# Kernel optimization log

Measured on AMD Instinct MI355X. Metric: run time of the kernel, lower is better.

## Reference

```python
import jax, jax.numpy as jnp
import numpy as np

N = 100000
E = 1600000
D = 64
N_LAYERS = 2


def setup_inputs() -> dict:
    key = jax.random.key(0)
    ks = jax.random.split(key, 4 + 4 * N_LAYERS)
    h = jax.random.normal(ks[0], (N, D), dtype=jnp.float32)
    x = jax.random.normal(ks[1], (N, 3), dtype=jnp.float32)
    edge_index = jax.random.randint(ks[2], (2, E), 0, N, dtype=jnp.int64)
    node_mask = jnp.ones((N, 1), dtype=jnp.float32)
    scale = 1.0 / np.sqrt(D)
    params = {}
    for i in range(N_LAYERS):
        params[f'W1_{i}'] = jax.random.normal(ks[4 + 4 * i], (D, D), dtype=jnp.float32) * scale
        params[f'b1_{i}'] = jax.random.normal(ks[5 + 4 * i], (D,), dtype=jnp.float32) * scale
        params[f'W2_{i}'] = jax.random.normal(ks[6 + 4 * i], (D, D), dtype=jnp.float32) * scale
        params[f'b2_{i}'] = jax.random.normal(ks[7 + 4 * i], (D,), dtype=jnp.float32) * scale
    return dict(h=h, x=x, edge_index=edge_index, node_mask=node_mask, **params)


def _gin_layer(h, src, dst, W1, b1, W2, b2):
    # GINConv with eps=0: mlp(h_i + sum_{j->i} h_j)
    agg = jax.ops.segment_sum(h[src], dst, num_segments=N)  # [N, D]
    z = h + agg
    z = jax.nn.relu(z @ W1 + b1)
    return z @ W2 + b2


def reference(h, x, edge_index, node_mask,
              W1_0, b1_0, W2_0, b2_0,
              W1_1, b1_1, W2_1, b2_1):
    src, dst = edge_index[0], edge_index[1]
    h = _gin_layer(h, src, dst, W1_0, b1_0, W2_0, b2_0)
    h = _gin_layer(h, src, dst, W1_1, b1_1, W2_1, b2_1)
    h = h * node_mask
    return (h, x)
```

## Files before the change

kernel.cpp:

```cpp
#include <hip/hip_runtime.h>


#define NN 100000
#define EE 1600000
#define CAP 48
#define NBIN 1024
#define BINCAP 2688
#define CHB 6250
#define OVF_CAPN 8000

#define OVFC_OFF   1024
#define OVF_OFF    1026
#define CNT_OFF    19200
#define BUCK_OFF   119296
#define BINNED_OFF 4919296
#define HB_OFF     4919296
#define PW_OFF     8119328

typedef __attribute__((ext_vector_type(8))) short s8v;
typedef __attribute__((ext_vector_type(4))) float f4v;

union U8 { unsigned u[4]; s8v s; };

static __device__ __forceinline__ unsigned short f2bf(float f) {
  unsigned u = __float_as_uint(f);
  return (unsigned short)((u + 0x7FFF + ((u >> 16) & 1)) >> 16);
}
static __device__ __forceinline__ float bf2f(unsigned short s) {
  return __uint_as_float(((unsigned)s) << 16);
}
static __device__ __forceinline__ unsigned pk2(float lo, float hi) {
  return (unsigned)f2bf(lo) | ((unsigned)f2bf(hi) << 16);
}

__global__ __launch_bounds__(256) void setup_k(const float* __restrict__ W1a,
                                               const float* __restrict__ W2a,
                                               const float* __restrict__ W1b,
                                               const float* __restrict__ W2b,
                                               unsigned short* __restrict__ pw,
                                               int* __restrict__ wsp) {
  const int t = threadIdx.x;
#pragma unroll
  for (int i = t; i < NBIN; i += 256) wsp[i] = i * BINCAP;
  if (t == 0) wsp[OVFC_OFF] = 0;
  const float* Ws[4] = {W1a, W2a, W1b, W2b};
#pragma unroll
  for (int m = 0; m < 4; ++m) {
    const float* __restrict__ W = Ws[m];
#pragma unroll 1
    for (int i = 0; i < 16; ++i) {
      const int e = i * 256 + t;
      const int j = e & 7;
      const int lv = (e >> 3) & 63;
      const int ks = (e >> 9) & 1;
      const int tt = e >> 10;
      const int k = ks * 32 + (lv >> 4) * 8 + j;
      const int n = tt * 16 + (lv & 15);
      pw[m * 4096 + e] = f2bf(W[k * 64 + n]);
    }
  }
}

__global__ __launch_bounds__(256) void scatter_k(const int* __restrict__ src,
                                                 const int* __restrict__ dst,
                                                 int* __restrict__ gcur,
                                                 int* __restrict__ binned,
                                                 int* __restrict__ ovf) {
  __shared__ int hist[NBIN], base[NBIN], lcnt[NBIN];
  const int t = threadIdx.x;
#pragma unroll
  for (int b = t; b < NBIN; b += 256) { hist[b] = 0; lcnt[b] = 0; }
  __syncthreads();
  const int s = blockIdx.x * CHB;
#pragma unroll 1
  for (int p = t; p < CHB / 2; p += 256) {
    const int2 dd = *reinterpret_cast<const int2*>(dst + s + 2 * p);
    atomicAdd(&hist[dd.x >> 7], 1);
    atomicAdd(&hist[dd.y >> 7], 1);
  }
  __syncthreads();
#pragma unroll
  for (int b = t; b < NBIN; b += 256) {
    const int c = hist[b];
    base[b] = c ? atomicAdd(&gcur[b], c) : 0;
  }
  __syncthreads();
#pragma unroll 1
  for (int p = t; p < CHB / 2; p += 256) {
    const int i = s + 2 * p;
    const int2 dd = *reinterpret_cast<const int2*>(dst + i);
    const int2 ss = *reinterpret_cast<const int2*>(src + i);
    {
      const int bin = dd.x >> 7;
      const int slot = base[bin] + atomicAdd(&lcnt[bin], 1);
      if (slot < (bin + 1) * BINCAP) {
        binned[slot] = ((dd.x & 127) << 17) | ss.x;
      } else {
        const int q = atomicAdd(&ovf[-2], 1);
        if (q < OVF_CAPN) { ovf[2 * q] = dd.x; ovf[2 * q + 1] = ss.x; }
      }
    }
    {
      const int bin = dd.y >> 7;
      const int slot = base[bin] + atomicAdd(&lcnt[bin], 1);
      if (slot < (bin + 1) * BINCAP) {
        binned[slot] = ((dd.y & 127) << 17) | ss.y;
      } else {
        const int q = atomicAdd(&ovf[-2], 1);
        if (q < OVF_CAPN) { ovf[2 * q] = dd.y; ovf[2 * q + 1] = ss.y; }
      }
    }
  }
}

__global__ __launch_bounds__(256) void bucketize_k(const int* __restrict__ gcur,
                                                   const int* __restrict__ binned,
                                                   int* __restrict__ bucket,
                                                   int* __restrict__ cnt,
                                                   int* __restrict__ ovf) {
  __shared__ int c128[128];
  const int t = threadIdx.x;
  const int bin = blockIdx.x;
  const int nbase = bin << 7;
  if (t < 128) c128[t] = 0;
  __syncthreads();
  const int s0 = bin * BINCAP;
  const int s1 = min(gcur[bin], s0 + BINCAP);
#pragma unroll 1
  for (int i = s0 + t; i < s1; i += 256) {
    const int p = binned[i];
    const int dlow = p >> 17;
    const int sv = p & 131071;
    const int slot = atomicAdd(&c128[dlow], 1);
    if (slot < CAP) {
      bucket[(nbase + dlow) * CAP + slot] = sv;
    } else {
      const int q = atomicAdd(&ovf[-2], 1);
      if (q < OVF_CAPN) { ovf[2 * q] = nbase + dlow; ovf[2 * q + 1] = sv; }
    }
  }
  __syncthreads();
  if (t < 128 && nbase + t < NN) {
    const int dc = min(c128[t], CAP);
    cnt[nbase + t] = c128[t];
    const int pad = min((dc + 15) & ~15, CAP);
    int* __restrict__ brow = bucket + (nbase + t) * CAP;
#pragma unroll 1
    for (int q2 = dc; q2 < pad; ++q2) brow[q2] = NN;
  }
}

__global__ __launch_bounds__(256) void cvtx_k(const float* __restrict__ h,
                                              unsigned* __restrict__ hb,
                                              const float* __restrict__ x,
                                              float* __restrict__ ox) {
  const int b = blockIdx.x;
  const int t = threadIdx.x;
  if (b < 3125) {
    const int i = b * 256 + t;
    const float4* __restrict__ h4 = reinterpret_cast<const float4*>(h);
    const float4 a = h4[2 * i], c = h4[2 * i + 1];
    uint4 o;
    o.x = pk2(a.x, a.y); o.y = pk2(a.z, a.w);
    o.z = pk2(c.x, c.y); o.w = pk2(c.z, c.w);
    reinterpret_cast<uint4*>(hb)[i] = o;
  } else {
    if (b == 3125 && t < 32) hb[NN * 32 + t] = 0;
    const int i = (b - 3125) * 256 + t;
    if (i < (NN * 3) / 4)
      reinterpret_cast<float4*>(ox)[i] = reinterpret_cast<const float4*>(x)[i];
  }
}

__global__ __launch_bounds__(256) void agg_k(const unsigned short* __restrict__ hb,
                                             const int* __restrict__ cnt,
                                             const int* __restrict__ bucket,
                                             unsigned* __restrict__ zbu) {
  const int l = threadIdx.x & 63;
  const int s = l >> 4, g = l & 15;
  int nb = blockIdx.x * 8 + (threadIdx.x >> 6) * 2;
  nb = __builtin_amdgcn_readfirstlane(nb);
  const int n0 = nb, n1 = nb + 1;

  const int2 c2 = *reinterpret_cast<const int2*>(cnt + n0);
  const int deg0 = min(c2.x, CAP), deg1 = min(c2.y, CAP);
  const int nit0 = (deg0 + 15) >> 4, nit1 = (deg1 + 15) >> 4;
  const int nc = min(nit0, nit1);

  const int4* __restrict__ br0 = reinterpret_cast<const int4*>(bucket + n0 * CAP);
  const int4* __restrict__ br1 = reinterpret_cast<const int4*>(bucket + n1 * CAP);
  const uint2* __restrict__ h2 = reinterpret_cast<const uint2*>(hb);

  const uint2 sv0 = h2[n0 * 16 + g];
  const uint2 sv1 = h2[n1 * 16 + g];
  const unsigned p00 = (s == 0) ? sv0.x : 0u, p01 = (s == 0) ? sv0.y : 0u;
  const unsigned p10 = (s == 0) ? sv1.x : 0u, p11 = (s == 0) ? sv1.y : 0u;
  float a0 = __uint_as_float(p00 << 16), a1 = __uint_as_float(p00 & 0xffff0000u);
  float a2 = __uint_as_float(p01 << 16), a3 = __uint_as_float(p01 & 0xffff0000u);
  float b0 = __uint_as_float(p10 << 16), b1 = __uint_as_float(p10 & 0xffff0000u);
  float b2 = __uint_as_float(p11 << 16), b3 = __uint_as_float(p11 & 0xffff0000u);

#define ACCA(vv)                                   \
    a0 += __uint_as_float(vv.x << 16);             \
    a1 += __uint_as_float(vv.x & 0xffff0000u);     \
    a2 += __uint_as_float(vv.y << 16);             \
    a3 += __uint_as_float(vv.y & 0xffff0000u);
#define ACCB(vv)                                   \
    b0 += __uint_as_float(vv.x << 16);             \
    b1 += __uint_as_float(vv.x & 0xffff0000u);     \
    b2 += __uint_as_float(vv.y << 16);             \
    b3 += __uint_as_float(vv.y & 0xffff0000u);

#pragma unroll 1
  for (int it = 0; it < nc; ++it) {
    const int4 q0 = br0[it * 4 + s];
    const int4 q1 = br1[it * 4 + s];
    const uint2 v0 = h2[q0.x * 16 + g];
    const uint2 v1 = h2[q0.y * 16 + g];
    const uint2 v2 = h2[q0.z * 16 + g];
    const uint2 v3 = h2[q0.w * 16 + g];
    const uint2 w0 = h2[q1.x * 16 + g];
    const uint2 w1 = h2[q1.y * 16 + g];
    const uint2 w2 = h2[q1.z * 16 + g];
    const uint2 w3 = h2[q1.w * 16 + g];
    ACCA(v0) ACCA(v1) ACCA(v2) ACCA(v3)
    ACCB(w0) ACCB(w1) ACCB(w2) ACCB(w3)
  }
#pragma unroll 1
  for (int it = nc; it < nit0; ++it) {
    const int4 q0 = br0[it * 4 + s];
    const uint2 v0 = h2[q0.x * 16 + g];
    const uint2 v1 = h2[q0.y * 16 + g];
    const uint2 v2 = h2[q0.z * 16 + g];
    const uint2 v3 = h2[q0.w * 16 + g];
    ACCA(v0) ACCA(v1) ACCA(v2) ACCA(v3)
  }
#pragma unroll 1
  for (int it = nc; it < nit1; ++it) {
    const int4 q1 = br1[it * 4 + s];
    const uint2 w0 = h2[q1.x * 16 + g];
    const uint2 w1 = h2[q1.y * 16 + g];
    const uint2 w2 = h2[q1.z * 16 + g];
    const uint2 w3 = h2[q1.w * 16 + g];
    ACCB(w0) ACCB(w1) ACCB(w2) ACCB(w3)
  }
#undef ACCA
#undef ACCB

  a0 += __shfl_xor(a0, 16); a1 += __shfl_xor(a1, 16);
  a2 += __shfl_xor(a2, 16); a3 += __shfl_xor(a3, 16);
  a0 += __shfl_xor(a0, 32); a1 += __shfl_xor(a1, 32);
  a2 += __shfl_xor(a2, 32); a3 += __shfl_xor(a3, 32);
  b0 += __shfl_xor(b0, 16); b1 += __shfl_xor(b1, 16);
  b2 += __shfl_xor(b2, 16); b3 += __shfl_xor(b3, 16);
  b0 += __shfl_xor(b0, 32); b1 += __shfl_xor(b1, 32);
  b2 += __shfl_xor(b2, 32); b3 += __shfl_xor(b3, 32);

  if (s == 0) {
    uint2 o0, o1;
    o0.x = pk2(a0, a1); o0.y = pk2(a2, a3);
    o1.x = pk2(b0, b1); o1.y = pk2(b2, b3);
    reinterpret_cast<uint2*>(zbu)[n0 * 32 + g] = o0;
    reinterpret_cast<uint2*>(zbu)[n1 * 32 + g] = o1;
  }
}

__global__ __launch_bounds__(256) void ovf_fix_k(const unsigned short* __restrict__ hb,
                                                 char* __restrict__ zb,
                                                 const int* __restrict__ ovfCnt,
                                                 const int* __restrict__ ovf) {
  const int cv = min(ovfCnt[0], OVF_CAPN);
  const int l = threadIdx.x & 63;
  const int w = threadIdx.x >> 6;
  for (int p = w; p < cv; p += 4) {
    const int d = ovf[2 * p];
    const int s = ovf[2 * p + 1];
    const float add = bf2f(hb[(s << 6) | l]);
    unsigned* wp = reinterpret_cast<unsigned*>(zb + d * 256 + (l >> 1) * 4);
    const bool hi = l & 1;
    unsigned cur = atomicAdd(wp, 0u);
    while (true) {
      const unsigned short hv = hi ? (unsigned short)(cur >> 16) : (unsigned short)(cur & 0xffffu);
      const unsigned short nh = f2bf(bf2f(hv) + add);
      const unsigned nw = hi ? ((cur & 0x0000ffffu) | ((unsigned)nh << 16))
                             : ((cur & 0xffff0000u) | (unsigned)nh);
      const unsigned prev = atomicCAS(wp, cur, nw);
      if (prev == cur) break;
      cur = prev;
    }
  }
}

template <int OUTBF>
__global__ __launch_bounds__(256) void mlp_mfma_k(
    const char* __restrict__ zb,
    void* __restrict__ hout,
    const unsigned short* __restrict__ pw1, const float* __restrict__ b1,
    const unsigned short* __restrict__ pw2, const float* __restrict__ b2,
    const float* __restrict__ mask) {
  __shared__ unsigned ldsu[128 * 33];
  const int tid = threadIdx.x;
  const int w = tid >> 6, l = tid & 63, g = l >> 4, mi = l & 15;
  const int m0 = blockIdx.x * 128;
  const int rbase = w * 32;

  s8v zf[2][2];
#pragma unroll
  for (int tm = 0; tm < 2; ++tm) {
    const int node = m0 + rbase + tm * 16 + mi;
    const int nc = node < NN ? node : NN - 1;
#pragma unroll
    for (int ks = 0; ks < 2; ++ks)
      zf[tm][ks] = *reinterpret_cast<const s8v*>(zb + nc * 256 + (ks * 32 + g * 8) * 2);
  }

  f4v acc[4][2];
#pragma unroll
  for (int t = 0; t < 4; ++t) {
    const f4v bv = *reinterpret_cast<const f4v*>(b1 + t * 16 + g * 4);
    acc[t][0] = bv; acc[t][1] = bv;
  }
#pragma unroll
  for (int t = 0; t < 4; ++t) {
#pragma unroll
    for (int ks = 0; ks < 2; ++ks) {
      const s8v wf = *reinterpret_cast<const s8v*>(pw1 + ((t * 2 + ks) * 64 + l) * 8);
#pragma unroll
      for (int tm = 0; tm < 2; ++tm)
        acc[t][tm] = __builtin_amdgcn_mfma_f32_16x16x32_bf16(wf, zf[tm][ks], acc[t][tm], 0, 0, 0);
    }
  }

#pragma unroll
  for (int t = 0; t < 4; ++t) {
#pragma unroll
    for (int tm = 0; tm < 2; ++tm) {
      const f4v a = acc[t][tm];
      const int row = rbase + tm * 16 + mi;
      const int base = row * 33 + t * 8 + g * 2;
      ldsu[base]     = pk2(fmaxf(a.x, 0.f), fmaxf(a.y, 0.f));
      ldsu[base + 1] = pk2(fmaxf(a.z, 0.f), fmaxf(a.w, 0.f));
    }
  }
  __syncthreads();

  s8v cf[2][2];
#pragma unroll
  for (int tm = 0; tm < 2; ++tm) {
    const int row = rbase + tm * 16 + mi;
#pragma unroll
    for (int ks = 0; ks < 2; ++ks) {
      const int b0 = row * 33 + ks * 16 + g * 4;
      U8 u8;
      u8.u[0] = ldsu[b0 + 0];
      u8.u[1] = ldsu[b0 + 1];
      u8.u[2] = ldsu[b0 + 2];
      u8.u[3] = ldsu[b0 + 3];
      cf[tm][ks] = u8.s;
    }
  }

  f4v acc2[4][2];
#pragma unroll
  for (int t = 0; t < 4; ++t) {
    const f4v bv = *reinterpret_cast<const f4v*>(b2 + t * 16 + g * 4);
    acc2[t][0] = bv; acc2[t][1] = bv;
  }
#pragma unroll
  for (int t = 0; t < 4; ++t) {
#pragma unroll
    for (int ks = 0; ks < 2; ++ks) {
      const s8v wf = *reinterpret_cast<const s8v*>(pw2 + ((t * 2 + ks) * 64 + l) * 8);
#pragma unroll
      for (int tm = 0; tm < 2; ++tm)
        acc2[t][tm] = __builtin_amdgcn_mfma_f32_16x16x32_bf16(wf, cf[tm][ks], acc2[t][tm], 0, 0, 0);
    }
  }

  if (OUTBF) {
    unsigned* __restrict__ ho = reinterpret_cast<unsigned*>(hout);
#pragma unroll
    for (int tm = 0; tm < 2; ++tm) {
      const int node = m0 + rbase + tm * 16 + mi;
      if (node < NN) {
#pragma unroll
        for (int t = 0; t < 4; ++t) {
          const f4v a = acc2[t][tm];
          const int idx = node * 32 + t * 8 + g * 2;
          uint2 p;
          p.x = pk2(a.x, a.y);
          p.y = pk2(a.z, a.w);
          *reinterpret_cast<uint2*>(&ho[idx]) = p;
        }
      }
    }
  } else {
    float* __restrict__ fo = reinterpret_cast<float*>(hout);
#pragma unroll
    for (int tm = 0; tm < 2; ++tm) {
      const int node = m0 + rbase + tm * 16 + mi;
      if (node < NN) {
        const float mv = mask[node];
#pragma unroll
        for (int t = 0; t < 4; ++t) {
          f4v v = acc2[t][tm];
          v *= mv;
          *reinterpret_cast<f4v*>(fo + node * 64 + t * 16 + g * 4) = v;
        }
      }
    }
  }
}

extern "C" void kernel_launch(void* const* d_in, const int* in_sizes, int n_in,
                              void* d_out, int out_size, void* d_ws, size_t ws_size,
                              hipStream_t stream) {
  (void)in_sizes; (void)n_in; (void)out_size; (void)ws_size;
  const float* h    = (const float*)d_in[0];
  const float* x    = (const float*)d_in[1];
  const int*   ei   = (const int*)d_in[2];
  const float* mask = (const float*)d_in[3];
  const float* W1_0 = (const float*)d_in[4];
  const float* b1_0 = (const float*)d_in[5];
  const float* W2_0 = (const float*)d_in[6];
  const float* b2_0 = (const float*)d_in[7];
  const float* W1_1 = (const float*)d_in[8];
  const float* b1_1 = (const float*)d_in[9];
  const float* W2_1 = (const float*)d_in[10];
  const float* b2_1 = (const float*)d_in[11];
  float* out = (float*)d_out;

  const int* src = ei;
  const int* dst = ei + EE;

  int* wsp       = (int*)d_ws;
  int* gcur      = wsp;
  int* ovfCnt    = wsp + OVFC_OFF;
  int* ovf       = wsp + OVF_OFF;
  int* cnt       = wsp + CNT_OFF;
  int* bucket    = wsp + BUCK_OFF;
  int* binned    = wsp + BINNED_OFF;
  unsigned* hb   = (unsigned*)(wsp + HB_OFF);
  unsigned short* pw = (unsigned short*)(wsp + PW_OFF);
  const unsigned short* hbs = (const unsigned short*)hb;
  unsigned* zbu  = (unsigned*)d_out;
  char* zb       = (char*)d_out;

  setup_k<<<1, 256, 0, stream>>>(W1_0, W2_0, W1_1, W2_1, pw, wsp);
  scatter_k<<<256, 256, 0, stream>>>(src, dst, gcur, binned, ovf);
  bucketize_k<<<782, 256, 0, stream>>>(gcur, binned, bucket, cnt, ovf);

  cvtx_k<<<3418, 256, 0, stream>>>(h, hb, x, out + NN * 64);

  agg_k<<<12500, 256, 0, stream>>>(hbs, cnt, bucket, zbu);
  ovf_fix_k<<<1, 256, 0, stream>>>(hbs, zb, ovfCnt, ovf);
  mlp_mfma_k<1><<<782, 256, 0, stream>>>(zb, hb, pw, b1_0, pw + 4096, b2_0, nullptr);

  agg_k<<<12500, 256, 0, stream>>>(hbs, cnt, bucket, zbu);
  ovf_fix_k<<<1, 256, 0, stream>>>(hbs, zb, ovfCnt, ovf);
  mlp_mfma_k<0><<<782, 256, 0, stream>>>(zb, out, pw + 8192, b1_1, pw + 12288, b2_1, mask);
}
```

Before: 146.1 us.

## Process four nodes per wave in aggregation and fold overflow fixup into it

Result: slower. 150.3 us (+2.9%).

```diff
diff --git a/kernel.cpp b/kernel.cpp
--- a/kernel.cpp
+++ b/kernel.cpp
@@ -175,30 +175,44 @@
 __global__ __launch_bounds__(256) void agg_k(const unsigned short* __restrict__ hb,
                                              const int* __restrict__ cnt,
                                              const int* __restrict__ bucket,
-                                             unsigned* __restrict__ zbu) {
+                                             unsigned* __restrict__ zbu,
+                                             const int* __restrict__ ovfCnt,
+                                             const int* __restrict__ ovf) {
   const int l = threadIdx.x & 63;
   const int s = l >> 4, g = l & 15;
-  int nb = blockIdx.x * 8 + (threadIdx.x >> 6) * 2;
+  int nb = blockIdx.x * 16 + (threadIdx.x >> 6) * 4;
   nb = __builtin_amdgcn_readfirstlane(nb);
-  const int n0 = nb, n1 = nb + 1;
-
-  const int2 c2 = *reinterpret_cast<const int2*>(cnt + n0);
-  const int deg0 = min(c2.x, CAP), deg1 = min(c2.y, CAP);
-  const int nit0 = (deg0 + 15) >> 4, nit1 = (deg1 + 15) >> 4;
-  const int nc = min(nit0, nit1);
+  const int n0 = nb, n1 = nb + 1, n2 = nb + 2, n3 = nb + 3;
+
+  const int4 c4 = *reinterpret_cast<const int4*>(cnt + nb);
+  const int nit0 = (min(c4.x, CAP) + 15) >> 4;
+  const int nit1 = (min(c4.y, CAP) + 15) >> 4;
+  const int nit2 = (min(c4.z, CAP) + 15) >> 4;
+  const int nit3 = (min(c4.w, CAP) + 15) >> 4;
+  const int nc = min(min(nit0, nit1), min(nit2, nit3));
 
   const int4* __restrict__ br0 = reinterpret_cast<const int4*>(bucket + n0 * CAP);
   const int4* __restrict__ br1 = reinterpret_cast<const int4*>(bucket + n1 * CAP);
+  const int4* __restrict__ br2 = reinterpret_cast<const int4*>(bucket + n2 * CAP);
+  const int4* __restrict__ br3 = reinterpret_cast<const int4*>(bucket + n3 * CAP);
   const uint2* __restrict__ h2 = reinterpret_cast<const uint2*>(hb);
 
-  const uint2 sv0 = h2[n0 * 16 + g];
-  const uint2 sv1 = h2[n1 * 16 + g];
-  const unsigned p00 = (s == 0) ? sv0.x : 0u, p01 = (s == 0) ? sv0.y : 0u;
-  const unsigned p10 = (s == 0) ? sv1.x : 0u, p11 = (s == 0) ? sv1.y : 0u;
-  float a0 = __uint_as_float(p00 << 16), a1 = __uint_as_float(p00 & 0xffff0000u);
-  float a2 = __uint_as_float(p01 << 16), a3 = __uint_as_float(p01 & 0xffff0000u);
-  float b0 = __uint_as_float(p10 << 16), b1 = __uint_as_float(p10 & 0xffff0000u);
-  float b2 = __uint_as_float(p11 << 16), b3 = __uint_as_float(p11 & 0xffff0000u);
+  const uint2 s0v = h2[n0 * 16 + g];
+  const uint2 s1v = h2[n1 * 16 + g];
+  const uint2 s2v = h2[n2 * 16 + g];
+  const uint2 s3v = h2[n3 * 16 + g];
+  const unsigned z0 = (s == 0) ? s0v.x : 0u, z1 = (s == 0) ? s0v.y : 0u;
+  const unsigned z2 = (s == 0) ? s1v.x : 0u, z3 = (s == 0) ? s1v.y : 0u;
+  const unsigned z4 = (s == 0) ? s2v.x : 0u, z5 = (s == 0) ? s2v.y : 0u;
+  const unsigned z6 = (s == 0) ? s3v.x : 0u, z7 = (s == 0) ? s3v.y : 0u;
+  float a0 = __uint_as_float(z0 << 16), a1 = __uint_as_float(z0 & 0xffff0000u);
+  float a2 = __uint_as_float(z1 << 16), a3 = __uint_as_float(z1 & 0xffff0000u);
+  float b0 = __uint_as_float(z2 << 16), b1 = __uint_as_float(z2 & 0xffff0000u);
+  float b2 = __uint_as_float(z3 << 16), b3 = __uint_as_float(z3 & 0xffff0000u);
+  float c0 = __uint_as_float(z4 << 16), c1 = __uint_as_float(z4 & 0xffff0000u);
+  float c2 = __uint_as_float(z5 << 16), c3 = __uint_as_float(z5 & 0xffff0000u);
+  float d0 = __uint_as_float(z6 << 16), d1 = __uint_as_float(z6 & 0xffff0000u);
+  float d2 = __uint_as_float(z7 << 16), d3 = __uint_as_float(z7 & 0xffff0000u);
 
 #define ACCA(vv)                                   \
     a0 += __uint_as_float(vv.x << 16);             \
@@ -210,11 +224,23 @@
     b1 += __uint_as_float(vv.x & 0xffff0000u);     \
     b2 += __uint_as_float(vv.y << 16);             \
     b3 += __uint_as_float(vv.y & 0xffff0000u);
+#define ACCC(vv)                                   \
+    c0 += __uint_as_float(vv.x << 16);             \
+    c1 += __uint_as_float(vv.x & 0xffff0000u);     \
+    c2 += __uint_as_float(vv.y << 16);             \
+    c3 += __uint_as_float(vv.y & 0xffff0000u);
+#define ACCD(vv)                                   \
+    d0 += __uint_as_float(vv.x << 16);             \
+    d1 += __uint_as_float(vv.x & 0xffff0000u);     \
+    d2 += __uint_as_float(vv.y << 16);             \
+    d3 += __uint_as_float(vv.y & 0xffff0000u);
 
 #pragma unroll 1
   for (int it = 0; it < nc; ++it) {
     const int4 q0 = br0[it * 4 + s];
     const int4 q1 = br1[it * 4 + s];
+    const int4 q2 = br2[it * 4 + s];
+    const int4 q3 = br3[it * 4 + s];
     const uint2 v0 = h2[q0.x * 16 + g];
     const uint2 v1 = h2[q0.y * 16 + g];
     const uint2 v2 = h2[q0.z * 16 + g];
@@ -223,8 +249,18 @@
     const uint2 w1 = h2[q1.y * 16 + g];
     const uint2 w2 = h2[q1.z * 16 + g];
     const uint2 w3 = h2[q1.w * 16 + g];
+    const uint2 x0 = h2[q2.x * 16 + g];
+    const uint2 x1 = h2[q2.y * 16 + g];
+    const uint2 x2 = h2[q2.z * 16 + g];
+    const uint2 x3 = h2[q2.w * 16 + g];
+    const uint2 y0 = h2[q3.x * 16 + g];
+    const uint2 y1 = h2[q3.y * 16 + g];
+    const uint2 y2 = h2[q3.z * 16 + g];
+    const uint2 y3 = h2[q3.w * 16 + g];
     ACCA(v0) ACCA(v1) ACCA(v2) ACCA(v3)
     ACCB(w0) ACCB(w1) ACCB(w2) ACCB(w3)
+    ACCC(x0) ACCC(x1) ACCC(x2) ACCC(x3)
+    ACCD(y0) ACCD(y1) ACCD(y2) ACCD(y3)
   }
 #pragma unroll 1
   for (int it = nc; it < nit0; ++it) {
@@ -244,8 +280,24 @@
     const uint2 w3 = h2[q1.w * 16 + g];
     ACCB(w0) ACCB(w1) ACCB(w2) ACCB(w3)
   }
-#undef ACCA
-#undef ACCB
+#pragma unroll 1
+  for (int it = nc; it < nit2; ++it) {
+    const int4 q2 = br2[it * 4 + s];
+    const uint2 x0 = h2[q2.x * 16 + g];
+    const uint2 x1 = h2[q2.y * 16 + g];
+    const uint2 x2 = h2[q2.z * 16 + g];
+    const uint2 x3 = h2[q2.w * 16 + g];
+    ACCC(x0) ACCC(x1) ACCC(x2) ACCC(x3)
+  }
+#pragma unroll 1
+  for (int it = nc; it < nit3; ++it) {
+    const int4 q3 = br3[it * 4 + s];
+    const uint2 y0 = h2[q3.x * 16 + g];
+    const uint2 y1 = h2[q3.y * 16 + g];
+    const uint2 y2 = h2[q3.z * 16 + g];
+    const uint2 y3 = h2[q3.w * 16 + g];
+    ACCD(y0) ACCD(y1) ACCD(y2) ACCD(y3)
+  }
 
   a0 += __shfl_xor(a0, 16); a1 += __shfl_xor(a1, 16);
   a2 += __shfl_xor(a2, 16); a3 += __shfl_xor(a3, 16);
@@ -255,40 +307,49 @@
   b2 += __shfl_xor(b2, 16); b3 += __shfl_xor(b3, 16);
   b0 += __shfl_xor(b0, 32); b1 += __shfl_xor(b1, 32);
   b2 += __shfl_xor(b2, 32); b3 += __shfl_xor(b3, 32);
+  c0 += __shfl_xor(c0, 16); c1 += __shfl_xor(c1, 16);
+  c2 += __shfl_xor(c2, 16); c3 += __shfl_xor(c3, 16);
+  c0 += __shfl_xor(c0, 32); c1 += __shfl_xor(c1, 32);
+  c2 += __shfl_xor(c2, 32); c3 += __shfl_xor(c3, 32);
+  d0 += __shfl_xor(d0, 16); d1 += __shfl_xor(d1, 16);
+  d2 += __shfl_xor(d2, 16); d3 += __shfl_xor(d3, 16);
+  d0 += __shfl_xor(d0, 32); d1 += __shfl_xor(d1, 32);
+  d2 += __shfl_xor(d2, 32); d3 += __shfl_xor(d3, 32);
+
+  const int cv = min(ovfCnt[0], OVF_CAPN);
+  if (cv > 0) {
+#pragma unroll 1
+    for (int p = 0; p < cv; ++p) {
+      const int d = ovf[2 * p];
+      if (d >= n0 && d <= n3) {
+        const uint2 vv = h2[ovf[2 * p + 1] * 16 + g];
+        const float e0 = __uint_as_float(vv.x << 16);
+        const float e1 = __uint_as_float(vv.x & 0xffff0000u);
+        const float e2 = __uint_as_float(vv.y << 16);
+        const float e3 = __uint_as_float(vv.y & 0xffff0000u);
+        if (d == n0)      { a0 += e0; a1 += e1; a2 += e2; a3 += e3; }
+        else if (d == n1) { b0 += e0; b1 += e1; b2 += e2; b3 += e3; }
+        else if (d == n2) { c0 += e0; c1 += e1; c2 += e2; c3 += e3; }
+        else              { d0 += e0; d1 += e1; d2 += e2; d3 += e3; }
+      }
+    }
+  }
 
   if (s == 0) {
-    uint2 o0, o1;
-    o0.x = pk2(a0, a1); o0.y = pk2(a2, a3);
-    o1.x = pk2(b0, b1); o1.y = pk2(b2, b3);
-    reinterpret_cast<uint2*>(zbu)[n0 * 32 + g] = o0;
-    reinterpret_cast<uint2*>(zbu)[n1 * 32 + g] = o1;
-  }
-}
-
-__global__ __launch_bounds__(256) void ovf_fix_k(const unsigned short* __restrict__ hb,
-                                                 char* __restrict__ zb,
-                                                 const int* __restrict__ ovfCnt,
-                                                 const int* __restrict__ ovf) {
-  const int cv = min(ovfCnt[0], OVF_CAPN);
-  const int l = threadIdx.x & 63;
-  const int w = threadIdx.x >> 6;
-  for (int p = w; p < cv; p += 4) {
-    const int d = ovf[2 * p];
-    const int s = ovf[2 * p + 1];
-    const float add = bf2f(hb[(s << 6) | l]);
-    unsigned* wp = reinterpret_cast<unsigned*>(zb + d * 256 + (l >> 1) * 4);
-    const bool hi = l & 1;
-    unsigned cur = atomicAdd(wp, 0u);
-    while (true) {
-      const unsigned short hv = hi ? (unsigned short)(cur >> 16) : (unsigned short)(cur & 0xffffu);
-      const unsigned short nh = f2bf(bf2f(hv) + add);
-      const unsigned nw = hi ? ((cur & 0x0000ffffu) | ((unsigned)nh << 16))
-                             : ((cur & 0xffff0000u) | (unsigned)nh);
-      const unsigned prev = atomicCAS(wp, cur, nw);
-      if (prev == cur) break;
-      cur = prev;
-    }
-  }
+    uint2 o;
+    o.x = pk2(a0, a1); o.y = pk2(a2, a3);
+    reinterpret_cast<uint2*>(zbu)[n0 * 32 + g] = o;
+    o.x = pk2(b0, b1); o.y = pk2(b2, b3);
+    reinterpret_cast<uint2*>(zbu)[n1 * 32 + g] = o;
+    o.x = pk2(c0, c1); o.y = pk2(c2, c3);
+    reinterpret_cast<uint2*>(zbu)[n2 * 32 + g] = o;
+    o.x = pk2(d0, d1); o.y = pk2(d2, d3);
+    reinterpret_cast<uint2*>(zbu)[n3 * 32 + g] = o;
+  }
+#undef ACCA
+#undef ACCB
+#undef ACCC
+#undef ACCD
 }
 
 template <int OUTBF>
@@ -452,11 +513,9 @@
 
   cvtx_k<<<3418, 256, 0, stream>>>(h, hb, x, out + NN * 64);
 
-  agg_k<<<12500, 256, 0, stream>>>(hbs, cnt, bucket, zbu);
-  ovf_fix_k<<<1, 256, 0, stream>>>(hbs, zb, ovfCnt, ovf);
+  agg_k<<<6250, 256, 0, stream>>>(hbs, cnt, bucket, zbu, ovfCnt, ovf);
   mlp_mfma_k<1><<<782, 256, 0, stream>>>(zb, hb, pw, b1_0, pw + 4096, b2_0, nullptr);
 
-  agg_k<<<12500, 256, 0, stream>>>(hbs, cnt, bucket, zbu);
-  ovf_fix_k<<<1, 256, 0, stream>>>(hbs, zb, ovfCnt, ovf);
+  agg_k<<<6250, 256, 0, stream>>>(hbs, cnt, bucket, zbu, ovfCnt, ovf);
   mlp_mfma_k<0><<<782, 256, 0, stream>>>(zb, out, pw + 8192, b1_1, pw + 12288, b2_1, mask);
 }
```
